# Kernel optimization log

Measured on AMD Instinct MI355X. Metric: run time of the kernel, lower is better.

Reference implementation:

```python
import jax, jax.numpy as jnp
import numpy as np

B, T, C, HD = 16, 2048, 1024, 64


def setup_inputs() -> dict:
    key = jax.random.key(0)
    kx, kk, kq, kv = jax.random.split(key, 4)
    x = jax.random.normal(kx, (B, T, C), dtype=jnp.float32)
    Wk = jax.random.normal(kk, (C, HD), dtype=jnp.float32) * (C ** -0.5)
    Wq = jax.random.normal(kq, (C, HD), dtype=jnp.float32) * (C ** -0.5)
    Wv = jax.random.normal(kv, (C, HD), dtype=jnp.float32) * (C ** -0.5)
    return {"x": x, "Wk": Wk, "Wq": Wq, "Wv": Wv}


def reference(x, Wk, Wq, Wv):
    Bs, Ts, Cs = x.shape
    k = x @ Wk  # [B,T,HD]
    q = x @ Wq
    v = x @ Wv
    # Faithful to original: scores = key @ query^T, scaled by 1/sqrt(C) (embed dim!)
    scores = jnp.einsum('bth,bsh->bts', k, q) / jnp.sqrt(jnp.float32(Cs))
    causal = jnp.tril(jnp.ones((Ts, Ts), dtype=bool))  # tril[:T,:T]
    scores = jnp.where(causal, scores, -jnp.inf)
    weights = jax.nn.softmax(scores, axis=-1)  # [B,T,T]
    return jnp.einsum('bts,bsh->bth', weights, v)  # [B,T,HD]
```

## Files before the change

kernel.cpp:

```cpp
#include <hip/hip_runtime.h>
#include <hip/hip_bf16.h>

#define B_ 16
#define T_ 2048
#define C_ 1024
#define HD_ 64

typedef __attribute__((ext_vector_type(8))) short bf16x8;
typedef __attribute__((ext_vector_type(4))) float f32x4;

__device__ __forceinline__ unsigned short f2bf(float f) {
  return __builtin_bit_cast(unsigned short, __float2bfloat16(f));
}

__device__ __forceinline__ bf16x8 cvt8(float4 a, float4 b) {
  bf16x8 r;
  r[0] = (short)f2bf(a.x); r[1] = (short)f2bf(a.y);
  r[2] = (short)f2bf(a.z); r[3] = (short)f2bf(a.w);
  r[4] = (short)f2bf(b.x); r[5] = (short)f2bf(b.y);
  r[6] = (short)f2bf(b.z); r[7] = (short)f2bf(b.w);
  return r;
}

__global__ void wconv_kernel(const float* __restrict__ Wk, const float* __restrict__ Wq,
                             const float* __restrict__ Wv, unsigned short* __restrict__ w3) {
  int o = blockIdx.x * 256 + threadIdx.x;
  if (o >= 16 * 12288) return;
  int kk = o / 12288;
  int n = o - kk * 12288;
  int row = n >> 6;
  int c = (n >> 3) & 7;
  int e = n & 7;
  int k = kk * 64 + (((c ^ (row & 7)) << 3) | e);
  int m = row >> 6, d = row & 63;
  const float* W = (m == 0) ? Wk : (m == 1) ? Wq : Wv;
  float v = W[k * HD_ + d];
  if (m == 0) v *= 0.03125f * 1.44269504088896f;
  w3[o] = f2bf(v);
}

__global__ __launch_bounds__(256, 3) void qkv_kernel(const float* __restrict__ x,
                                                     const unsigned short* __restrict__ w3,
                                                     unsigned short* __restrict__ kb,
                                                     unsigned short* __restrict__ qb,
                                                     unsigned short* __restrict__ vb) {
  __shared__ __align__(16) unsigned short wl[2 * 12288];

  const int tid = threadIdx.x;
  const int lane = tid & 63;
  const int w = tid >> 6;
  const int rh = w >> 1, ch = w & 1;
  const int l15 = lane & 15, lh = lane >> 4;
  const int r0 = blockIdx.x * 32;

  const float* xq = x + (size_t)(r0 + rh * 16 + l15) * C_ + lh * 8;
  const int fb0 = (ch * 96 + l15) * 64 + ((lh ^ (l15 & 7)) << 3);
  const int fb1 = (ch * 96 + l15) * 64 + (((4 | lh) ^ (l15 & 7)) << 3);

  f32x4 acc[6];
#pragma unroll
  for (int i = 0; i < 6; ++i) acc[i] = {0.f, 0.f, 0.f, 0.f};

  float4 xa0, xa1, xa2, xa3, xb0, xb1, xb2, xb3;

#define STAGE(BUF, WS)                                                              \
  do {                                                                              \
    _Pragma("unroll")                                                               \
    for (int i_ = 0; i_ < 6; ++i_) {                                                \
      const int idx_ = i_ * 256 + tid;                                              \
      __builtin_amdgcn_global_load_lds(                                             \
          (const __attribute__((address_space(1))) void*)((WS) + idx_ * 8),         \
          (__attribute__((address_space(3))) void*)&wl[(BUF) * 12288 + idx_ * 8],   \
          16, 0, 0);                                                                \
    }                                                                               \
  } while (0)

#define XLOADA(P) do { const float* p_ = (P);                                  \
    xa0 = *(const float4*)(p_);      xa1 = *(const float4*)(p_ + 4);           \
    xa2 = *(const float4*)(p_ + 32); xa3 = *(const float4*)(p_ + 36); } while (0)
#define XLOADB(P) do { const float* p_ = (P);                                  \
    xb0 = *(const float4*)(p_);      xb1 = *(const float4*)(p_ + 4);           \
    xb2 = *(const float4*)(p_ + 32); xb3 = *(const float4*)(p_ + 36); } while (0)

#define COMPUTE(BUF, X0, X1, X2, X3)                                                \
  do {                                                                              \
    bf16x8 a0 = cvt8(X0, X1);                                                       \
    bf16x8 a1 = cvt8(X2, X3);                                                       \
    _Pragma("unroll")                                                               \
    for (int f_ = 0; f_ < 6; ++f_) {                                                \
      bf16x8 b0 = *(const bf16x8*)&wl[(BUF) * 12288 + f_ * 1024 + fb0];             \
      acc[f_] = __builtin_amdgcn_mfma_f32_16x16x32_bf16(a0, b0, acc[f_], 0, 0, 0);  \
      bf16x8 b1 = *(const bf16x8*)&wl[(BUF) * 12288 + f_ * 1024 + fb1];             \
      acc[f_] = __builtin_amdgcn_mfma_f32_16x16x32_bf16(a1, b1, acc[f_], 0, 0, 0);  \
    }                                                                               \
  } while (0)

#define SB __builtin_amdgcn_sched_barrier(0)
#define WAIT(VM)                                                  \
  do {                                                            \
    SB;                                                           \
    asm volatile("s_waitcnt vmcnt(" #VM ")" ::: "memory");        \
    SB;                                                           \
    __builtin_amdgcn_s_barrier();                                 \
  } while (0)

  const unsigned short* ws = w3;
  STAGE(0, ws);
  ws += 12288;
  XLOADA(xq);

#pragma unroll 1
  for (int it = 0; it < 7; ++it) {
    STAGE(1, ws);
    ws += 12288;
    XLOADB(xq + 64);
    WAIT(10);
    COMPUTE(0, xa0, xa1, xa2, xa3);
    __builtin_amdgcn_s_barrier();
    STAGE(0, ws);
    ws += 12288;
    XLOADA(xq + 128);
    WAIT(10);
    COMPUTE(1, xb0, xb1, xb2, xb3);
    __builtin_amdgcn_s_barrier();
    xq += 128;
  }
  STAGE(1, ws);
  XLOADB(xq + 64);
  WAIT(10);
  COMPUTE(0, xa0, xa1, xa2, xa3);
  __builtin_amdgcn_s_barrier();
  WAIT(0);
  COMPUTE(1, xb0, xb1, xb2, xb3);

#undef WAIT
#undef SB
#undef COMPUTE
#undef XLOADB
#undef XLOADA
#undef STAGE

#pragma unroll
  for (int rr = 0; rr < 4; ++rr) {
    size_t row = (size_t)(r0 + rh * 16 + lh * 4 + rr);
    if (ch == 0) {
#pragma unroll
      for (int f = 0; f < 4; ++f)
        kb[row * HD_ + f * 16 + l15] = f2bf(acc[f][rr]);
      qb[row * HD_ + 0 + l15]  = f2bf(acc[4][rr]);
      qb[row * HD_ + 16 + l15] = f2bf(acc[5][rr]);
    } else {
      qb[row * HD_ + 32 + l15] = f2bf(acc[0][rr]);
      qb[row * HD_ + 48 + l15] = f2bf(acc[1][rr]);
#pragma unroll
      for (int f = 2; f < 6; ++f)
        vb[row * HD_ + (f - 2) * 16 + l15] = f2bf(acc[f][rr]);
    }
  }
}

__global__ __launch_bounds__(256) void attn_kernel(const unsigned short* __restrict__ kb,
                                                   const unsigned short* __restrict__ qb,
                                                   const unsigned short* __restrict__ vb,
                                                   float* __restrict__ out) {
  __shared__ __align__(16) unsigned short q_lds[2][64 * 72];
  __shared__ __align__(16) unsigned short v_lds[2][64 * 72];
  __shared__ __align__(16) unsigned short p_lds[64 * 72];

  const int tid = threadIdx.x;
  const int lane = tid & 63;
  const int w = tid >> 6;
  const int bid = blockIdx.x;
  const int idx = bid >> 4;
  const int jt = (idx < 16) ? (31 - idx) : (idx - 16);
  const int b = bid & 15;
  const int t0 = jt * 64;
  const int l15 = lane & 15;
  const int lh = lane >> 4;
  const size_t base = (size_t)b * T_ * HD_;

  const int qrow = tid >> 3, qc8 = tid & 7;
  const int vss = tid & 63, vd0 = (tid >> 6) * 8;

  bf16x8 kf[2];
#pragma unroll
  for (int ks = 0; ks < 2; ++ks)
    kf[ks] = *reinterpret_cast<const bf16x8*>(
        &kb[base + (size_t)(t0 + w * 16 + l15) * HD_ + ks * 32 + lh * 8]);

  bf16x8 qr0, qr1, vr0, vr1;
  qr0 = *reinterpret_cast<const bf16x8*>(&qb[base + (size_t)qrow * HD_ + qc8 * 8]);
  qr1 = *reinterpret_cast<const bf16x8*>(&qb[base + (size_t)(qrow + 32) * HD_ + qc8 * 8]);
  vr0 = *reinterpret_cast<const bf16x8*>(&vb[base + (size_t)vss * HD_ + vd0]);
  vr1 = *reinterpret_cast<const bf16x8*>(&vb[base + (size_t)vss * HD_ + vd0 + 32]);

  f32x4 o[4];
#pragma unroll
  for (int i = 0; i < 4; ++i) o[i] = {0.f, 0.f, 0.f, 0.f};
  float mrun[4], lrun[4];
#pragma unroll
  for (int r = 0; r < 4; ++r) { mrun[r] = -1e30f; lrun[r] = 0.f; }

  for (int j = 0; j <= jt; ++j) {
    const int buf = j & 1;
    *reinterpret_cast<bf16x8*>(&q_lds[buf][qrow * 72 + qc8 * 8]) = qr0;
    *reinterpret_cast<bf16x8*>(&q_lds[buf][(qrow + 32) * 72 + qc8 * 8]) = qr1;
#pragma unroll
    for (int jj = 0; jj < 8; ++jj) v_lds[buf][(vd0 + jj) * 72 + vss] = (unsigned short)vr0[jj];
#pragma unroll
    for (int jj = 0; jj < 8; ++jj) v_lds[buf][(vd0 + 32 + jj) * 72 + vss] = (unsigned short)vr1[jj];
    __syncthreads();

    if (j < jt) {
      const size_t sb = base + (size_t)(j + 1) * 64 * HD_;
      qr0 = *reinterpret_cast<const bf16x8*>(&qb[sb + (size_t)qrow * HD_ + qc8 * 8]);
      qr1 = *reinterpret_cast<const bf16x8*>(&qb[sb + (size_t)(qrow + 32) * HD_ + qc8 * 8]);
      vr0 = *reinterpret_cast<const bf16x8*>(&vb[sb + (size_t)vss * HD_ + vd0]);
      vr1 = *reinterpret_cast<const bf16x8*>(&vb[sb + (size_t)vss * HD_ + vd0 + 32]);
    }
    __builtin_amdgcn_sched_barrier(0);

    f32x4 sf[4];
#pragma unroll
    for (int cf = 0; cf < 4; ++cf) sf[cf] = {0.f, 0.f, 0.f, 0.f};
    __builtin_amdgcn_s_setprio(1);
#pragma unroll
    for (int ks = 0; ks < 2; ++ks) {
#pragma unroll
      for (int cf = 0; cf < 4; ++cf) {
        bf16x8 bq = *reinterpret_cast<const bf16x8*>(&q_lds[buf][(cf * 16 + l15) * 72 + ks * 32 + lh * 8]);
        sf[cf] = __builtin_amdgcn_mfma_f32_16x16x32_bf16(kf[ks], bq, sf[cf], 0, 0, 0);
      }
    }
    __builtin_amdgcn_s_setprio(0);

    const bool diag = (j == jt);
    const int s0 = j * 64;
    float pv[4][4];
#pragma unroll
    for (int r = 0; r < 4; ++r) {
      const int tg = t0 + w * 16 + lh * 4 + r;
      float pm = -1e30f;
#pragma unroll
      for (int cf = 0; cf < 4; ++cf) {
        float v = sf[cf][r];
        if (diag && (s0 + cf * 16 + l15) > tg) v = -1e30f;
        pv[cf][r] = v;
        pm = fmaxf(pm, v);
      }
      pm = fmaxf(pm, __shfl_xor(pm, 1));
      pm = fmaxf(pm, __shfl_xor(pm, 2));
      pm = fmaxf(pm, __shfl_xor(pm, 4));
      pm = fmaxf(pm, __shfl_xor(pm, 8));
      float mn = fmaxf(mrun[r], pm);
      float scl = exp2f(mrun[r] - mn);
      mrun[r] = mn;
      float rs = 0.f;
#pragma unroll
      for (int cf = 0; cf < 4; ++cf) {
        float e = exp2f(pv[cf][r] - mn);
        pv[cf][r] = e;
        rs += e;
      }
      rs += __shfl_xor(rs, 1);
      rs += __shfl_xor(rs, 2);
      rs += __shfl_xor(rs, 4);
      rs += __shfl_xor(rs, 8);
      lrun[r] = lrun[r] * scl + rs;
#pragma unroll
      for (int df = 0; df < 4; ++df) o[df][r] *= scl;
    }
#pragma unroll
    for (int cf = 0; cf < 4; ++cf)
#pragma unroll
      for (int r = 0; r < 4; ++r)
        p_lds[(w * 16 + lh * 4 + r) * 72 + cf * 16 + l15] = f2bf(pv[cf][r]);

    __builtin_amdgcn_s_setprio(1);
#pragma unroll
    for (int ks = 0; ks < 2; ++ks) {
      bf16x8 pa = *reinterpret_cast<const bf16x8*>(&p_lds[(w * 16 + l15) * 72 + ks * 32 + lh * 8]);
#pragma unroll
      for (int df = 0; df < 4; ++df) {
        bf16x8 bv = *reinterpret_cast<const bf16x8*>(&v_lds[buf][(df * 16 + l15) * 72 + ks * 32 + lh * 8]);
        o[df] = __builtin_amdgcn_mfma_f32_16x16x32_bf16(pa, bv, o[df], 0, 0, 0);
      }
    }
    __builtin_amdgcn_s_setprio(0);
  }

#pragma unroll
  for (int r = 0; r < 4; ++r) {
    float inv = 1.f / lrun[r];
    int row = t0 + w * 16 + lh * 4 + r;
#pragma unroll
    for (int df = 0; df < 4; ++df)
      out[base + (size_t)row * HD_ + df * 16 + l15] = o[df][r] * inv;
  }
}

extern "C" void kernel_launch(void* const* d_in, const int* in_sizes, int n_in,
                              void* d_out, int out_size, void* d_ws, size_t ws_size,
                              hipStream_t stream) {
  const float* x  = (const float*)d_in[0];
  const float* Wk = (const float*)d_in[1];
  const float* Wq = (const float*)d_in[2];
  const float* Wv = (const float*)d_in[3];
  float* out = (float*)d_out;

  char* ws = (char*)d_ws;
  unsigned short* w3 = (unsigned short*)ws;
  unsigned short* kb = (unsigned short*)(ws + 524288);
  unsigned short* qb = (unsigned short*)(ws + 524288 + 4 * 1024 * 1024);
  unsigned short* vb = (unsigned short*)(ws + 524288 + 8 * 1024 * 1024);

  hipLaunchKernelGGL(wconv_kernel, dim3(768), dim3(256), 0, stream, Wk, Wq, Wv, w3);
  hipLaunchKernelGGL(qkv_kernel, dim3(1024), dim3(256), 0, stream, x, w3, kb, qb, vb);
  hipLaunchKernelGGL(attn_kernel, dim3(512), dim3(256), 0, stream, kb, qb, vb, out);
}
```

Before: 112.6 us.

## Retile QKV projection to 128-row blocks with each wave computing all outputs

The QKV projection kernel now uses 512-thread blocks covering 128 rows instead of 256-thread blocks covering 32 rows. Each wave computes all 192 output columns (K, Q and V) for its 16 rows, so the staged weight tile in shared memory is reused by four times as many rows. This cuts redundant weight staging traffic and gives each wave its own x rows, removing the split where two waves loaded the same x row. In exchange there are more accumulator registers per wave and fewer blocks (256), which may underfill the GPU and lower occupancy.

```diff
diff --git a/kernel.cpp b/kernel.cpp
--- a/kernel.cpp
+++ b/kernel.cpp
@@ -39,7 +39,7 @@
   w3[o] = f2bf(v);
 }
 
-__global__ __launch_bounds__(256, 3) void qkv_kernel(const float* __restrict__ x,
+__global__ __launch_bounds__(512, 2) void qkv_kernel(const float* __restrict__ x,
                                                      const unsigned short* __restrict__ w3,
                                                      unsigned short* __restrict__ kb,
                                                      unsigned short* __restrict__ qb,
@@ -49,36 +49,35 @@
   const int tid = threadIdx.x;
   const int lane = tid & 63;
   const int w = tid >> 6;
-  const int rh = w >> 1, ch = w & 1;
   const int l15 = lane & 15, lh = lane >> 4;
-  const int r0 = blockIdx.x * 32;
-
-  const float* xq = x + (size_t)(r0 + rh * 16 + l15) * C_ + lh * 8;
-  const int fb0 = (ch * 96 + l15) * 64 + ((lh ^ (l15 & 7)) << 3);
-  const int fb1 = (ch * 96 + l15) * 64 + (((4 | lh) ^ (l15 & 7)) << 3);
-
-  f32x4 acc[6];
-#pragma unroll
-  for (int i = 0; i < 6; ++i) acc[i] = {0.f, 0.f, 0.f, 0.f};
+  const int r0 = blockIdx.x * 128;
+
+  const float* xp = x + (size_t)(r0 + w * 16 + l15) * C_ + lh * 8;
+  const int fb0 = l15 * 64 + ((lh ^ (l15 & 7)) << 3);
+  const int fb1 = l15 * 64 + (((4 | lh) ^ (l15 & 7)) << 3);
+
+  f32x4 acc[12];
+#pragma unroll
+  for (int i = 0; i < 12; ++i) acc[i] = {0.f, 0.f, 0.f, 0.f};
 
   float4 xa0, xa1, xa2, xa3, xb0, xb1, xb2, xb3;
 
-#define STAGE(BUF, WS)                                                              \
+#define STAGE(BUF, KK)                                                              \
   do {                                                                              \
     _Pragma("unroll")                                                               \
-    for (int i_ = 0; i_ < 6; ++i_) {                                                \
-      const int idx_ = i_ * 256 + tid;                                              \
+    for (int i_ = 0; i_ < 3; ++i_) {                                                \
+      const int eo_ = ((w * 3 + i_) << 9) + lane * 8;    \
       __builtin_amdgcn_global_load_lds(                                             \
-          (const __attribute__((address_space(1))) void*)((WS) + idx_ * 8),         \
-          (__attribute__((address_space(3))) void*)&wl[(BUF) * 12288 + idx_ * 8],   \
+          (const __attribute__((address_space(1))) void*)(w3 + (KK) * 12288 + eo_), \
+          (__attribute__((address_space(3))) void*)&wl[(BUF) * 12288 + eo_],        \
           16, 0, 0);                                                                \
     }                                                                               \
   } while (0)
 
-#define XLOADA(P) do { const float* p_ = (P);                                  \
+#define XLOADA(KK) do { const float* p_ = xp + (KK) * 64;                      \
     xa0 = *(const float4*)(p_);      xa1 = *(const float4*)(p_ + 4);           \
     xa2 = *(const float4*)(p_ + 32); xa3 = *(const float4*)(p_ + 36); } while (0)
-#define XLOADB(P) do { const float* p_ = (P);                                  \
+#define XLOADB(KK) do { const float* p_ = xp + (KK) * 64;                      \
     xb0 = *(const float4*)(p_);      xb1 = *(const float4*)(p_ + 4);           \
     xb2 = *(const float4*)(p_ + 32); xb3 = *(const float4*)(p_ + 36); } while (0)
 
@@ -87,7 +86,7 @@
     bf16x8 a0 = cvt8(X0, X1);                                                       \
     bf16x8 a1 = cvt8(X2, X3);                                                       \
     _Pragma("unroll")                                                               \
-    for (int f_ = 0; f_ < 6; ++f_) {                                                \
+    for (int f_ = 0; f_ < 12; ++f_) {                                               \
       bf16x8 b0 = *(const bf16x8*)&wl[(BUF) * 12288 + f_ * 1024 + fb0];             \
       acc[f_] = __builtin_amdgcn_mfma_f32_16x16x32_bf16(a0, b0, acc[f_], 0, 0, 0);  \
       bf16x8 b1 = *(const bf16x8*)&wl[(BUF) * 12288 + f_ * 1024 + fb1];             \
@@ -104,30 +103,31 @@
     __builtin_amdgcn_s_barrier();                                 \
   } while (0)
 
-  const unsigned short* ws = w3;
-  STAGE(0, ws);
-  ws += 12288;
-  XLOADA(xq);
+  STAGE(0, 0);
+  SB;
+  XLOADA(0);
+  SB;
 
 #pragma unroll 1
   for (int it = 0; it < 7; ++it) {
-    STAGE(1, ws);
-    ws += 12288;
-    XLOADB(xq + 64);
-    WAIT(10);
+    const int k2 = it * 2;
+    STAGE(1, k2 + 1);
+    SB;
+    XLOADB(k2 + 1);
+    WAIT(7);
     COMPUTE(0, xa0, xa1, xa2, xa3);
     __builtin_amdgcn_s_barrier();
-    STAGE(0, ws);
-    ws += 12288;
-    XLOADA(xq + 128);
-    WAIT(10);
+    STAGE(0, k2 + 2);
+    SB;
+    XLOADA(k2 + 2);
+    WAIT(7);
     COMPUTE(1, xb0, xb1, xb2, xb3);
     __builtin_amdgcn_s_barrier();
-    xq += 128;
   }
-  STAGE(1, ws);
-  XLOADB(xq + 64);
-  WAIT(10);
+  STAGE(1, 15);
+  SB;
+  XLOADB(15);
+  WAIT(7);
   COMPUTE(0, xa0, xa1, xa2, xa3);
   __builtin_amdgcn_s_barrier();
   WAIT(0);
@@ -141,20 +141,14 @@
 #undef STAGE
 
 #pragma unroll
-  for (int rr = 0; rr < 4; ++rr) {
-    size_t row = (size_t)(r0 + rh * 16 + lh * 4 + rr);
-    if (ch == 0) {
-#pragma unroll
-      for (int f = 0; f < 4; ++f)
-        kb[row * HD_ + f * 16 + l15] = f2bf(acc[f][rr]);
-      qb[row * HD_ + 0 + l15]  = f2bf(acc[4][rr]);
-      qb[row * HD_ + 16 + l15] = f2bf(acc[5][rr]);
-    } else {
-      qb[row * HD_ + 32 + l15] = f2bf(acc[0][rr]);
-      qb[row * HD_ + 48 + l15] = f2bf(acc[1][rr]);
-#pragma unroll
-      for (int f = 2; f < 6; ++f)
-        vb[row * HD_ + (f - 2) * 16 + l15] = f2bf(acc[f][rr]);
+  for (int cf = 0; cf < 4; ++cf) {
+    int col = cf * 16 + l15;
+#pragma unroll
+    for (int r = 0; r < 4; ++r) {
+      size_t row = (size_t)(r0 + w * 16 + lh * 4 + r);
+      kb[row * HD_ + col] = f2bf(acc[cf][r]);
+      qb[row * HD_ + col] = f2bf(acc[4 + cf][r]);
+      vb[row * HD_ + col] = f2bf(acc[8 + cf][r]);
     }
   }
 }
@@ -315,6 +309,6 @@
   unsigned short* vb = (unsigned short*)(ws + 524288 + 8 * 1024 * 1024);
 
   hipLaunchKernelGGL(wconv_kernel, dim3(768), dim3(256), 0, stream, Wk, Wq, Wv, w3);
-  hipLaunchKernelGGL(qkv_kernel, dim3(1024), dim3(256), 0, stream, x, w3, kb, qb, vb);
+  hipLaunchKernelGGL(qkv_kernel, dim3(256), dim3(512), 0, stream, x, w3, kb, qb, vb);
   hipLaunchKernelGGL(attn_kernel, dim3(512), dim3(256), 0, stream, kb, qb, vb, out);
 }
```

Result: faster. 97.96 us (-13.0%).
